# Kernel optimization log

Hardware: AMD Instinct MI355X
Metric: run time of the kernel (lower is better)

## Reference

```python
import jax, jax.numpy as jnp
import numpy as np

SHAPES = np.array([[64, 64], [32, 32], [16, 16], [8, 8]], dtype=np.int64)  # (H_l, W_l)
STARTS = np.array([0, 4096, 5120, 5376], dtype=np.int64)
N_HEADS, N_LEVELS, N_POINTS = 8, 4, 4
NUM_LAYERS, D_MODEL, D_FFN = 6, 256, 1024
B, S = 1, int(SHAPES[:, 0].dot(SHAPES[:, 1]).item()) if False else (1, 5440)[1]
B = 1


def setup_inputs():
    key = jax.random.key(0)
    ks = jax.random.split(key, 16)
    C, F, L = D_MODEL, D_FFN, NUM_LAYERS
    w = lambda k, shape, s: jax.random.normal(k, shape, jnp.float32) * s
    d = {}
    d["src"] = jax.random.normal(ks[0], (B, S, C), jnp.float32)
    d["pos"] = jax.random.normal(ks[1], (B, S, C), jnp.float32) * 0.1
    d["valid_ratios"] = jnp.ones((B, N_LEVELS, 2), jnp.float32)
    d["spatial_shapes"] = jnp.asarray(SHAPES)
    d["level_start_index"] = jnp.asarray(STARTS)
    d["Wv"] = w(ks[2], (L, C, C), 0.03); d["bv"] = jnp.zeros((L, C), jnp.float32)
    d["Woff"] = w(ks[3], (L, C, N_HEADS * N_LEVELS * N_POINTS * 2), 0.002)
    d["boff"] = w(ks[4], (L, N_HEADS * N_LEVELS * N_POINTS * 2), 0.5)
    d["Wattn"] = w(ks[5], (L, C, N_HEADS * N_LEVELS * N_POINTS), 0.02)
    d["battn"] = jnp.zeros((L, N_HEADS * N_LEVELS * N_POINTS), jnp.float32)
    d["Wout"] = w(ks[6], (L, C, C), 0.03); d["bout"] = jnp.zeros((L, C), jnp.float32)
    d["ln1_g"] = jnp.ones((L, C), jnp.float32); d["ln1_b"] = jnp.zeros((L, C), jnp.float32)
    d["W1"] = w(ks[7], (L, C, F), 0.03); d["b1"] = jnp.zeros((L, F), jnp.float32)
    d["W2"] = w(ks[8], (L, F, C), 0.03); d["b2"] = jnp.zeros((L, C), jnp.float32)
    d["ln2_g"] = jnp.ones((L, C), jnp.float32); d["ln2_b"] = jnp.zeros((L, C), jnp.float32)
    return d


def layer_norm(x, g, b, eps=1e-5):
    m = jnp.mean(x, -1, keepdims=True)
    v = jnp.mean(jnp.square(x - m), -1, keepdims=True)
    return (x - m) * jax.lax.rsqrt(v + eps) * g + b


def get_reference_points(valid_ratios):
    # returns [B, S, L, 2] (x, y) normalized coords, matching the TF while-loop
    refs = []
    for l in range(N_LEVELS):
        H, W = int(SHAPES[l, 0]), int(SHAPES[l, 1])
        ry = jnp.linspace(0.5, H - 0.5, H)
        rx = jnp.linspace(0.5, W - 0.5, W)
        yy, xx = jnp.meshgrid(ry, rx, indexing='ij')
        yn = yy.reshape(-1)[None, :] / (valid_ratios[:, l, 0:1] * H)
        xn = xx.reshape(-1)[None, :] / (valid_ratios[:, l, 1:2] * W)
        refs.append(jnp.stack([xn, yn], -1))  # [B, H*W, 2]
    ref = jnp.concatenate(refs, axis=1)       # [B, S, 2]
    vr_wh = valid_ratios[:, None, :, ::-1]    # [B, 1, L, 2] -> (w, h)
    return ref[:, :, None, :] * vr_wh


def bilinear_sample(v_l, loc, Hl, Wl):
    # v_l: [B, Hl*Wl, nH, Dh]; loc: [B, S, nH, P, 2] in [0,1] coords
    # grid_sample align_corners=False, zero padding: pix = loc*size - 0.5
    x = loc[..., 0] * Wl - 0.5
    y = loc[..., 1] * Hl - 0.5
    x0 = jnp.floor(x); y0 = jnp.floor(y)
    lx = x - x0; ly = y - y0
    x0i = x0.astype(jnp.int32); y0i = y0.astype(jnp.int32)
    b_idx = jnp.arange(v_l.shape[0])[:, None, None, None]
    h_idx = jnp.arange(v_l.shape[2])[None, None, :, None]

    def gather(xi, yi):
        valid = (xi >= 0) & (xi < Wl) & (yi >= 0) & (yi < Hl)
        idx = jnp.clip(yi, 0, Hl - 1) * Wl + jnp.clip(xi, 0, Wl - 1)
        v = v_l[b_idx, idx, h_idx, :]  # [B,S,nH,P,Dh]
        return v * valid[..., None].astype(v.dtype)

    v00 = gather(x0i, y0i); v01 = gather(x0i + 1, y0i)
    v10 = gather(x0i, y0i + 1); v11 = gather(x0i + 1, y0i + 1)
    w00 = (1 - lx) * (1 - ly); w01 = lx * (1 - ly)
    w10 = (1 - lx) * ly; w11 = lx * ly
    return (v00 * w00[..., None] + v01 * w01[..., None]
            + v10 * w10[..., None] + v11 * w11[..., None])


def msda(query, src, ref, Wv, bv, Woff, boff, Wattn, battn, Wout, bout):
    Bq, Sq, C = src.shape
    Dh = C // N_HEADS
    value = (src @ Wv + bv).reshape(Bq, Sq, N_HEADS, Dh)
    off = (query @ Woff + boff).reshape(Bq, Sq, N_HEADS, N_LEVELS, N_POINTS, 2)
    aw = jax.nn.softmax((query @ Wattn + battn)
                        .reshape(Bq, Sq, N_HEADS, N_LEVELS * N_POINTS), -1)
    aw = aw.reshape(Bq, Sq, N_HEADS, N_LEVELS, N_POINTS)
    normalizer = jnp.asarray(SHAPES[:, ::-1].copy(), jnp.float32)  # [L,2]=(W,H)
    loc = ref[:, :, None, :, None, :] + off / normalizer[None, None, None, :, None, :]
    out = jnp.zeros((Bq, Sq, N_HEADS, Dh), value.dtype)
    for l in range(N_LEVELS):
        Hl, Wl = int(SHAPES[l, 0]), int(SHAPES[l, 1])
        s0 = int(STARTS[l])
        v_l = value[:, s0:s0 + Hl * Wl]
        sampled = bilinear_sample(v_l, loc[:, :, :, l], Hl, Wl)  # [B,S,nH,P,Dh]
        out = out + jnp.einsum('bshpd,bshp->bshd', sampled, aw[:, :, :, l])
    return out.reshape(Bq, Sq, C) @ Wout + bout


def reference(src, pos, valid_ratios, spatial_shapes, level_start_index,
              Wv, bv, Woff, boff, Wattn, battn, Wout, bout,
              ln1_g, ln1_b, W1, b1, W2, b2, ln2_g, ln2_b):
    ref = get_reference_points(valid_ratios)
    x = src
    for i in range(NUM_LAYERS):
        a = msda(x + pos, x, ref, Wv[i], bv[i], Woff[i], boff[i],
                 Wattn[i], battn[i], Wout[i], bout[i])
        x = layer_norm(x + a, ln1_g[i], ln1_b[i])
        f = jax.nn.relu(x @ W1[i] + b1[i]) @ W2[i] + b2[i]
        x = layer_norm(x + f, ln2_g[i], ln2_b[i])
    return x
```

## Files before the change

### kernel.cpp

```cpp
#include <hip/hip_runtime.h>
#include <hip/hip_bf16.h>

#define S_TOT 5440
#define C_DIM 256
#define F_DIM 1024
#define N_LAYERS 6

__device__ __constant__ int c_HW[4]    = {64, 32, 16, 8};
__device__ __constant__ int c_logW[4]  = {6, 5, 4, 3};
__device__ __constant__ int c_start[4] = {0, 4096, 5120, 5376};

typedef __attribute__((ext_vector_type(8))) short bf16x8;
typedef __attribute__((ext_vector_type(4))) float f32x4;
typedef __attribute__((ext_vector_type(4))) unsigned int u32x4;

__device__ __forceinline__ short f2bf(float f) {
    __hip_bfloat16 h = __float2bfloat16(f);
    return *reinterpret_cast<short*>(&h);
}
union uf32 { unsigned int u; float f; };
__device__ __forceinline__ float lo_f(unsigned int u) { uf32 c; c.u = u << 16;          return c.f; }
__device__ __forceinline__ float hi_f(unsigned int u) { uf32 c; c.u = u & 0xffff0000u; return c.f; }

__global__ __launch_bounds__(256) void prep_weights(
    const float* __restrict__ Wv, const float* __restrict__ Woff,
    const float* __restrict__ Wattn, const float* __restrict__ Wout,
    const float* __restrict__ W1, const float* __restrict__ W2,
    unsigned short* __restrict__ WT)
{
    __shared__ short T[64][72];
    const int bid = blockIdx.x;
    const int layer = bid / 184;
    const int r = bid % 184;
    const float* src; unsigned short* dst; int K, N, kb, nb;
    if (r < 16)       { src = Wv    + (long)layer*65536;  dst = WT + 0       + (long)layer*65536;  K=256;  N=256;  kb=r&3;        nb=r>>2; }
    else if (r < 32)  { src = Woff  + (long)layer*65536;  dst = WT + 393216  + (long)layer*65536;  K=256;  N=256;  kb=(r-16)&3;   nb=(r-16)>>2; }
    else if (r < 40)  { src = Wattn + (long)layer*32768;  dst = WT + 786432  + (long)layer*32768;  K=256;  N=128;  kb=(r-32)&3;   nb=(r-32)>>2; }
    else if (r < 56)  { src = Wout  + (long)layer*65536;  dst = WT + 983040  + (long)layer*65536;  K=256;  N=256;  kb=(r-40)&3;   nb=(r-40)>>2; }
    else if (r < 120) { src = W1    + (long)layer*262144; dst = WT + 1376256 + (long)layer*262144; K=256;  N=1024; kb=(r-56)&3;   nb=(r-56)>>2; }
    else              { src = W2    + (long)layer*262144; dst = WT + 2949120 + (long)layer*262144; K=1024; N=256;  kb=(r-120)&15; nb=(r-120)>>4; }
    const int k0 = kb * 64, n0 = nb * 64;
    const int t = threadIdx.x;
    {
        const int row = t >> 2, cg = (t & 3) * 16;
        const float* sp = src + (long)(k0 + row) * N + n0 + cg;
        float4 v0 = *(const float4*)sp;
        float4 v1 = *(const float4*)(sp + 4);
        float4 v2 = *(const float4*)(sp + 8);
        float4 v3 = *(const float4*)(sp + 12);
        short tmp[16];
        tmp[0]=f2bf(v0.x); tmp[1]=f2bf(v0.y); tmp[2]=f2bf(v0.z); tmp[3]=f2bf(v0.w);
        tmp[4]=f2bf(v1.x); tmp[5]=f2bf(v1.y); tmp[6]=f2bf(v1.z); tmp[7]=f2bf(v1.w);
        tmp[8]=f2bf(v2.x); tmp[9]=f2bf(v2.y); tmp[10]=f2bf(v2.z); tmp[11]=f2bf(v2.w);
        tmp[12]=f2bf(v3.x); tmp[13]=f2bf(v3.y); tmp[14]=f2bf(v3.z); tmp[15]=f2bf(v3.w);
        *(bf16x8*)&T[row][cg]     = *(bf16x8*)&tmp[0];
        *(bf16x8*)&T[row][cg + 8] = *(bf16x8*)&tmp[8];
    }
    __syncthreads();
    {
        const int n = t >> 2, kg = (t & 3) * 16;
        short o[16];
        #pragma unroll
        for (int j = 0; j < 16; ++j) o[j] = T[kg + j][n];
        unsigned short* dp = dst + (long)(n0 + n) * K + k0 + kg;
        *(bf16x8*)dp       = *(bf16x8*)&o[0];
        *(bf16x8*)(dp + 8) = *(bf16x8*)&o[8];
    }
}

__device__ __forceinline__ void prep_A(
    const float* __restrict__ Ain, const float* __restrict__ g,
    const float* __restrict__ b, const float* __restrict__ pos,
    float* __restrict__ xout, int mBase, int doLN,
    short (*As)[264])
{
    const int t = threadIdx.x;
    const int row = t >> 2, q4 = t & 3;
    const long gbase = (long)(mBase + row) * 256 + q4 * 64;
    float va[64];
    #pragma unroll
    for (int j = 0; j < 16; ++j) {
        float4 v = *(const float4*)(Ain + gbase + j * 4);
        va[j*4+0] = v.x; va[j*4+1] = v.y; va[j*4+2] = v.z; va[j*4+3] = v.w;
    }
    if (doLN) {
        float s1 = 0.f, s2 = 0.f;
        #pragma unroll
        for (int j = 0; j < 64; ++j) { s1 += va[j]; s2 += va[j] * va[j]; }
        s1 += __shfl_xor(s1, 1); s2 += __shfl_xor(s2, 1);
        s1 += __shfl_xor(s1, 2); s2 += __shfl_xor(s2, 2);
        const float mean = s1 * (1.f / 256.f);
        const float var  = s2 * (1.f / 256.f) - mean * mean;
        const float rstd = rsqrtf(var + 1e-5f);
        #pragma unroll
        for (int j = 0; j < 16; ++j) {
            float4 g4 = *(const float4*)(g + q4 * 64 + j * 4);
            float4 b4 = *(const float4*)(b + q4 * 64 + j * 4);
            va[j*4+0] = (va[j*4+0] - mean) * rstd * g4.x + b4.x;
            va[j*4+1] = (va[j*4+1] - mean) * rstd * g4.y + b4.y;
            va[j*4+2] = (va[j*4+2] - mean) * rstd * g4.z + b4.z;
            va[j*4+3] = (va[j*4+3] - mean) * rstd * g4.w + b4.w;
        }
    }
    if (xout) {
        #pragma unroll
        for (int j = 0; j < 16; ++j) {
            float4 v;
            v.x = va[j*4+0]; v.y = va[j*4+1]; v.z = va[j*4+2]; v.w = va[j*4+3];
            *(float4*)(xout + gbase + j * 4) = v;
        }
    }
    if (pos) {
        #pragma unroll
        for (int j = 0; j < 16; ++j) {
            float4 p = *(const float4*)(pos + gbase + j * 4);
            va[j*4+0] += p.x; va[j*4+1] += p.y; va[j*4+2] += p.z; va[j*4+3] += p.w;
        }
    }
    #pragma unroll
    for (int j8 = 0; j8 < 8; ++j8) {
        short tmp[8];
        #pragma unroll
        for (int e = 0; e < 8; ++e) tmp[e] = f2bf(va[j8 * 8 + e]);
        *(bf16x8*)&As[row][q4 * 64 + j8 * 8] = *(bf16x8*)tmp;
    }
}

template<int NF>
__device__ __forceinline__ void core_Alds(
    const unsigned short* __restrict__ Bt, int nBase,
    const short (*As)[264], short (*Bs)[72], f32x4 (&acc)[2][NF])
{
    const int t = threadIdx.x;
    const int lane = t & 63, wave = t >> 6;
    const int wr = wave >> 1, wc = wave & 1;
    const int lr = lane & 15;

    #pragma unroll
    for (int i = 0; i < 2; ++i)
        #pragma unroll
        for (int j = 0; j < NF; ++j)
            acc[i][j] = (f32x4){0.f, 0.f, 0.f, 0.f};

    for (int k0 = 0; k0 < 256; k0 += 64) {
        bf16x8 rb[NF];
        #pragma unroll
        for (int q = 0; q < NF; ++q) {
            int flat = q * 256 + t, row = flat >> 3, cg = (flat & 7) * 8;
            rb[q] = *(const bf16x8*)(Bt + (long)(nBase + row) * 256 + k0 + cg);
        }
        __syncthreads();
        #pragma unroll
        for (int q = 0; q < NF; ++q) {
            int flat = q * 256 + t, row = flat >> 3, cg = (flat & 7) * 8;
            *(bf16x8*)&Bs[row][cg] = rb[q];
        }
        __syncthreads();
        #pragma unroll
        for (int kk = 0; kk < 2; ++kk) {
            const int lks = kk * 32 + (lane >> 4) * 8;
            bf16x8 af[2], bfr[NF];
            #pragma unroll
            for (int fm = 0; fm < 2; ++fm)
                af[fm] = *(const bf16x8*)&As[wr * 32 + fm * 16 + lr][k0 + lks];
            #pragma unroll
            for (int fn = 0; fn < NF; ++fn)
                bfr[fn] = *(bf16x8*)&Bs[wc * (NF * 16) + fn * 16 + lr][lks];
            #pragma unroll
            for (int fm = 0; fm < 2; ++fm)
                #pragma unroll
                for (int fn = 0; fn < NF; ++fn)
                    acc[fm][fn] = __builtin_amdgcn_mfma_f32_16x16x32_bf16(
                        af[fm], bfr[fn], acc[fm][fn], 0, 0, 0);
        }
    }
}

template<int NF>
__device__ __forceinline__ void gemm_core(
    const unsigned short* __restrict__ A, const unsigned short* __restrict__ Bt,
    int K, int mBase, int nBase, short (*As)[72], short (*Bs)[72],
    f32x4 (&acc)[2][NF])
{
    const int t = threadIdx.x;
    const int lane = t & 63, wave = t >> 6;
    const int wr = wave >> 1, wc = wave & 1;
    const int lr = lane & 15;

    #pragma unroll
    for (int i = 0; i < 2; ++i)
        #pragma unroll
        for (int j = 0; j < NF; ++j)
            acc[i][j] = (f32x4){0.f, 0.f, 0.f, 0.f};

    for (int k0 = 0; k0 < K; k0 += 64) {
        bf16x8 ra[2], rb[NF];
        #pragma unroll
        for (int q = 0; q < 2; ++q) {
            int flat = q * 256 + t, row = flat >> 3, cg = (flat & 7) * 8;
            ra[q] = *(const bf16x8*)(A + (long)(mBase + row) * K + k0 + cg);
        }
        #pragma unroll
        for (int q = 0; q < NF; ++q) {
            int flat = q * 256 + t, row = flat >> 3, cg = (flat & 7) * 8;
            rb[q] = *(const bf16x8*)(Bt + (long)(nBase + row) * K + k0 + cg);
        }
        __syncthreads();
        #pragma unroll
        for (int q = 0; q < 2; ++q) {
            int flat = q * 256 + t, row = flat >> 3, cg = (flat & 7) * 8;
            *(bf16x8*)&As[row][cg] = ra[q];
        }
        #pragma unroll
        for (int q = 0; q < NF; ++q) {
            int flat = q * 256 + t, row = flat >> 3, cg = (flat & 7) * 8;
            *(bf16x8*)&Bs[row][cg] = rb[q];
        }
        __syncthreads();
        #pragma unroll
        for (int kk = 0; kk < 2; ++kk) {
            const int lks = kk * 32 + (lane >> 4) * 8;
            bf16x8 af[2], bfr[NF];
            #pragma unroll
            for (int fm = 0; fm < 2; ++fm)
                af[fm] = *(bf16x8*)&As[wr * 32 + fm * 16 + lr][lks];
            #pragma unroll
            for (int fn = 0; fn < NF; ++fn)
                bfr[fn] = *(bf16x8*)&Bs[wc * (NF * 16) + fn * 16 + lr][lks];
            #pragma unroll
            for (int fm = 0; fm < 2; ++fm)
                #pragma unroll
                for (int fn = 0; fn < NF; ++fn)
                    acc[fm][fn] = __builtin_amdgcn_mfma_f32_16x16x32_bf16(
                        af[fm], bfr[fn], acc[fm][fn], 0, 0, 0);
        }
    }
}

__global__ __launch_bounds__(256) void proj_ln(
    const float* __restrict__ Ain, const float* __restrict__ pos,
    const float* __restrict__ g, const float* __restrict__ b,
    const unsigned short* __restrict__ WvT, const float* __restrict__ bv,
    const unsigned short* __restrict__ WofT, const float* __restrict__ bof,
    const unsigned short* __restrict__ WatT, const float* __restrict__ bat,
    unsigned short* __restrict__ value_bf, float* __restrict__ offraw,
    float* __restrict__ logits, float* __restrict__ xcur, int doLN)
{
    __shared__ short As[64][264];
    __shared__ short Bs[128][72];
    const int ny = blockIdx.y, mBase = blockIdx.x * 64;
    const unsigned short* Bp; const float* bias; int nBase, kind;
    if (ny < 2)      { Bp = WvT;  bias = bv;  nBase = ny * 128;       kind = 0; }
    else if (ny < 4) { Bp = WofT; bias = bof; nBase = (ny - 2) * 128; kind = 1; }
    else             { Bp = WatT; bias = bat; nBase = 0;              kind = 2; }

    prep_A(Ain, g, b, (kind > 0) ? pos : nullptr,
           (doLN && ny == 0) ? xcur : nullptr, mBase, doLN, As);

    f32x4 acc[2][4];
    core_Alds<4>(Bp, nBase, As, Bs, acc);

    const int lane = threadIdx.x & 63, wave = threadIdx.x >> 6;
    const int wr = wave >> 1, wc = wave & 1;
    #pragma unroll
    for (int fm = 0; fm < 2; ++fm)
        #pragma unroll
        for (int fn = 0; fn < 4; ++fn)
            #pragma unroll
            for (int r = 0; r < 4; ++r) {
                int m = mBase + wr * 32 + fm * 16 + (lane >> 4) * 4 + r;
                int n = nBase + wc * 64 + fn * 16 + (lane & 15);
                float v = acc[fm][fn][r] + bias[n];
                if (kind == 0)      value_bf[(long)m * 256 + n] = (unsigned short)f2bf(v);
                else if (kind == 1) offraw[(long)m * 256 + n] = v;
                else                logits[(long)m * 128 + n] = v;
            }
}

__global__ __launch_bounds__(256) void gemm_w1ln(
    const float* __restrict__ Ain, const float* __restrict__ g,
    const float* __restrict__ b, const unsigned short* __restrict__ W1T,
    const float* __restrict__ bias, unsigned short* __restrict__ hbuf,
    float* __restrict__ xout)
{
    __shared__ short As[64][264];
    __shared__ short Bs[128][72];
    const int mBase = blockIdx.x * 64, nBase = blockIdx.y * 128;

    prep_A(Ain, g, b, nullptr, (blockIdx.y == 0) ? xout : nullptr, mBase, 1, As);

    f32x4 acc[2][4];
    core_Alds<4>(W1T, nBase, As, Bs, acc);

    const int lane = threadIdx.x & 63, wave = threadIdx.x >> 6;
    const int wr = wave >> 1, wc = wave & 1;
    #pragma unroll
    for (int fm = 0; fm < 2; ++fm)
        #pragma unroll
        for (int fn = 0; fn < 4; ++fn)
            #pragma unroll
            for (int r = 0; r < 4; ++r) {
                int m = mBase + wr * 32 + fm * 16 + (lane >> 4) * 4 + r;
                int n = nBase + wc * 64 + fn * 16 + (lane & 15);
                float v = fmaxf(acc[fm][fn][r] + bias[n], 0.f);
                hbuf[(long)m * 1024 + n] = (unsigned short)f2bf(v);
            }
}

__global__ __launch_bounds__(256) void gemm_res(
    const unsigned short* __restrict__ A, const unsigned short* __restrict__ Bt,
    const float* __restrict__ bias, const float* __restrict__ res,
    float* __restrict__ out, int K)
{
    __shared__ short As[64][72];
    __shared__ short Bs[64][72];
    const int mBase = blockIdx.x * 64, nBase = blockIdx.y * 64;
    f32x4 acc[2][2];
    gemm_core<2>(A, Bt, K, mBase, nBase, As, Bs, acc);

    const int lane = threadIdx.x & 63, wave = threadIdx.x >> 6;
    const int wr = wave >> 1, wc = wave & 1;
    #pragma unroll
    for (int fm = 0; fm < 2; ++fm)
        #pragma unroll
        for (int fn = 0; fn < 2; ++fn)
            #pragma unroll
            for (int r = 0; r < 4; ++r) {
                int m = mBase + wr * 32 + fm * 16 + (lane >> 4) * 4 + r;
                int n = nBase + wc * 32 + fn * 16 + (lane & 15);
                out[(long)m * 256 + n] = acc[fm][fn][r] + bias[n] + res[(long)m * 256 + n];
            }
}

__global__ __launch_bounds__(256) void msda2(
    const unsigned short* __restrict__ value, const float* __restrict__ offraw,
    const float* __restrict__ logits, const float* __restrict__ vr,
    unsigned short* __restrict__ outB)
{
    const int t = threadIdx.x;
    const int q = t >> 7, tt = t & 127;
    const int s = blockIdx.x * 2 + q;

    __shared__ int4   sIdx[2][128];
    __shared__ float4 sW[2][128];

    {
        const int pt = tt & 15, l = pt >> 2;

        float lg = logits[(long)s * 128 + tt];
        float m = lg;
        #pragma unroll
        for (int o = 1; o < 16; o <<= 1) m = fmaxf(m, __shfl_xor(m, o));
        float e = expf(lg - m);
        float sum = e;
        #pragma unroll
        for (int o = 1; o < 16; o <<= 1) sum += __shfl_xor(sum, o);
        float aw = e / sum;

        int ls = (s < 4096) ? 0 : (s < 5120) ? 1 : (s < 5376) ? 2 : 3;
        int lw = c_logW[ls];
        int Wq = c_HW[ls];
        int rem = s - c_start[ls];
        int qi = rem >> lw, qj = rem & (Wq - 1);
        float xh = (qj + 0.5f) / (vr[ls * 2 + 1] * (float)Wq);
        float yh = (qi + 0.5f) / (vr[ls * 2 + 0] * (float)Wq);

        const int Wl = c_HW[l], sl = c_start[l];
        const float fW = (float)Wl;
        float refx = xh * vr[l * 2 + 1];
        float refy = yh * vr[l * 2 + 0];
        float2 oxy = *(const float2*)(offraw + (long)s * 256 + tt * 2);
        float x = refx * fW + oxy.x - 0.5f;
        float y = refy * fW + oxy.y - 0.5f;
        float x0f = floorf(x), y0f = floorf(y);
        float fx = x - x0f, fy = y - y0f;
        int x0 = (int)x0f, y0 = (int)y0f;
        int x1 = x0 + 1, y1 = y0 + 1;
        float vx0 = (x0 >= 0 && x0 < Wl) ? 1.f : 0.f;
        float vx1 = (x1 >= 0 && x1 < Wl) ? 1.f : 0.f;
        float vy0 = (y0 >= 0 && y0 < Wl) ? 1.f : 0.f;
        float vy1 = (y1 >= 0 && y1 < Wl) ? 1.f : 0.f;
        int cx0 = min(max(x0, 0), Wl - 1), cx1 = min(max(x1, 0), Wl - 1);
        int cy0 = min(max(y0, 0), Wl - 1), cy1 = min(max(y1, 0), Wl - 1);

        int4 id4;
        id4.x = sl + cy0 * Wl + cx0;
        id4.y = sl + cy0 * Wl + cx1;
        id4.z = sl + cy1 * Wl + cx0;
        id4.w = sl + cy1 * Wl + cx1;
        sIdx[q][tt] = id4;
        float4 w4;
        w4.x = aw * (1.f - fx) * (1.f - fy) * vx0 * vy0;
        w4.y = aw * fx * (1.f - fy) * vx1 * vy0;
        w4.z = aw * (1.f - fx) * fy * vx0 * vy1;
        w4.w = aw * fx * fy * vx1 * vy1;
        sW[q][tt] = w4;
    }
    __syncthreads();

    const int h = tt >> 4, pg = (tt >> 2) & 3, dq = tt & 3;
    const int cb = h * 32 + dq * 8;

    float a8[8] = {0.f,0.f,0.f,0.f,0.f,0.f,0.f,0.f};
    #pragma unroll
    for (int p = 0; p < 4; ++p) {
        const int ei = h * 16 + pg * 4 + p;
        int4 id = sIdx[q][ei];
        float4 w = sW[q][ei];
        u32x4 u0 = *(const u32x4*)(value + (long)id.x * 256 + cb);
        u32x4 u1 = *(const u32x4*)(value + (long)id.y * 256 + cb);
        u32x4 u2 = *(const u32x4*)(value + (long)id.z * 256 + cb);
        u32x4 u3 = *(const u32x4*)(value + (long)id.w * 256 + cb);
        #pragma unroll
        for (int j = 0; j < 4; ++j) {
            a8[2*j]   += w.x * lo_f(u0[j]) + w.y * lo_f(u1[j])
                       + w.z * lo_f(u2[j]) + w.w * lo_f(u3[j]);
            a8[2*j+1] += w.x * hi_f(u0[j]) + w.y * hi_f(u1[j])
                       + w.z * hi_f(u2[j]) + w.w * hi_f(u3[j]);
        }
    }
    #pragma unroll
    for (int j = 0; j < 8; ++j) {
        a8[j] += __shfl_xor(a8[j], 4);
        a8[j] += __shfl_xor(a8[j], 8);
    }
    if (pg == 0) {
        short o8[8];
        #pragma unroll
        for (int j = 0; j < 8; ++j) o8[j] = f2bf(a8[j]);
        *(bf16x8*)(outB + (long)s * 256 + cb) = *(bf16x8*)o8;
    }
}

__global__ __launch_bounds__(256) void ln4f(
    const float* __restrict__ in, const float* __restrict__ g,
    const float* __restrict__ b, float* __restrict__ out)
{
    const int wave = threadIdx.x >> 6, lane = threadIdx.x & 63;
    const int s = blockIdx.x * 4 + wave;
    f32x4 v = *(const f32x4*)(in + (long)s * 256 + lane * 4);

    float sum = v[0] + v[1] + v[2] + v[3];
    #pragma unroll
    for (int o = 1; o < 64; o <<= 1) sum += __shfl_xor(sum, o);
    const float mean = sum * (1.f / 256.f);

    f32x4 d = v - mean;
    float sq = d[0]*d[0] + d[1]*d[1] + d[2]*d[2] + d[3]*d[3];
    #pragma unroll
    for (int o = 1; o < 64; o <<= 1) sq += __shfl_xor(sq, o);
    const float rstd = rsqrtf(sq * (1.f / 256.f) + 1e-5f);

    f32x4 gg = *(const f32x4*)(g + lane * 4);
    f32x4 bb = *(const f32x4*)(b + lane * 4);
    f32x4 o4 = d * rstd * gg + bb;
    *(f32x4*)(out + (long)s * 256 + lane * 4) = o4;
}

extern "C" void kernel_launch(void* const* d_in, const int* in_sizes, int n_in,
                              void* d_out, int out_size, void* d_ws, size_t ws_size,
                              hipStream_t stream) {
    const float* src   = (const float*)d_in[0];
    const float* pos   = (const float*)d_in[1];
    const float* vr    = (const float*)d_in[2];
    const float* Wv    = (const float*)d_in[5];
    const float* bv    = (const float*)d_in[6];
    const float* Woff  = (const float*)d_in[7];
    const float* boff  = (const float*)d_in[8];
    const float* Wattn = (const float*)d_in[9];
    const float* battn = (const float*)d_in[10];
    const float* Wout  = (const float*)d_in[11];
    const float* bout  = (const float*)d_in[12];
    const float* ln1g  = (const float*)d_in[13];
    const float* ln1b  = (const float*)d_in[14];
    const float* W1    = (const float*)d_in[15];
    const float* b1    = (const float*)d_in[16];
    const float* W2    = (const float*)d_in[17];
    const float* b2    = (const float*)d_in[18];
    const float* ln2g  = (const float*)d_in[19];
    const float* ln2b  = (const float*)d_in[20];

    const int S = S_TOT, C = C_DIM;
    const long SC = (long)S * C;

    float* ws     = (float*)d_ws;
    float* tmp2   = ws;
    float* xcur   = tmp2 + SC;
    float* offraw = xcur + SC;
    float* logits = offraw + SC;
    unsigned short* value_bf = (unsigned short*)(logits + (long)S * 128);
    unsigned short* msda_bf  = value_bf + SC;
    unsigned short* hbuf_bf  = msda_bf + SC;
    unsigned short* WT       = hbuf_bf + (long)S * F_DIM;

    float* xln1 = offraw;

    const unsigned short* WvT  = WT + 0;
    const unsigned short* WofT = WT + 393216;
    const unsigned short* WatT = WT + 786432;
    const unsigned short* WouT = WT + 983040;
    const unsigned short* W1T  = WT + 1376256;
    const unsigned short* W2T  = WT + 2949120;

    prep_weights<<<1104, 256, 0, stream>>>(Wv, Woff, Wattn, Wout, W1, W2, WT);

    for (int i = 0; i < N_LAYERS; ++i) {
        const float* Ain = (i == 0) ? src : tmp2;
        const float* g2  = (i == 0) ? nullptr : ln2g + (long)(i - 1) * C;
        const float* bb2 = (i == 0) ? nullptr : ln2b + (long)(i - 1) * C;
        const float* resWout = (i == 0) ? src : xcur;

        proj_ln<<<dim3(85, 5), 256, 0, stream>>>(
            Ain, pos, g2, bb2,
            WvT + (long)i * 65536, bv + (long)i * C,
            WofT + (long)i * 65536, boff + (long)i * 256,
            WatT + (long)i * 32768, battn + (long)i * 128,
            value_bf, offraw, logits, xcur, (i == 0) ? 0 : 1);

        msda2<<<S / 2, 256, 0, stream>>>(value_bf, offraw, logits, vr, msda_bf);

        gemm_res<<<dim3(85, 4), 256, 0, stream>>>(
            msda_bf, WouT + (long)i * 65536, bout + (long)i * C, resWout, tmp2, 256);

        gemm_w1ln<<<dim3(85, 8), 256, 0, stream>>>(
            tmp2, ln1g + (long)i * C, ln1b + (long)i * C,
            W1T + (long)i * 262144, b1 + (long)i * F_DIM, hbuf_bf, xln1);

        gemm_res<<<dim3(85, 4), 256, 0, stream>>>(
            hbuf_bf, W2T + (long)i * 262144, b2 + (long)i * C, xln1, tmp2, 1024);
    }

    ln4f<<<S / 4, 256, 0, stream>>>(
        tmp2, ln2g + (long)(N_LAYERS - 1) * C, ln2b + (long)(N_LAYERS - 1) * C,
        (float*)d_out);
}
```

Baseline: 503.5 us.

## Store offsets and logits in bf16 and widen W1 GEMM tile to 256 columns

The projection kernel now writes sampling offsets and attention logits as bf16 instead of fp32, and the sampling kernel reads them back with bit-shift conversions. This halves the memory traffic for those intermediates, at the cost of lower precision in the sampling offsets. Separately, the W1 GEMM tile grows from 128 to 256 columns, which halves the grid and the redundant LayerNorm prep of the A tile. The larger tile raises registers and LDS per block, which may reduce occupancy. The workspace is re-laid out so xln1 has its own buffer instead of aliasing offraw.

```diff
diff --git a/kernel.cpp b/kernel.cpp
--- a/kernel.cpp
+++ b/kernel.cpp
@@ -21,6 +21,7 @@
 union uf32 { unsigned int u; float f; };
 __device__ __forceinline__ float lo_f(unsigned int u) { uf32 c; c.u = u << 16;          return c.f; }
 __device__ __forceinline__ float hi_f(unsigned int u) { uf32 c; c.u = u & 0xffff0000u; return c.f; }
+__device__ __forceinline__ float bf2f(unsigned short u) { uf32 c; c.u = ((unsigned int)u) << 16; return c.f; }
 
 __global__ __launch_bounds__(256) void prep_weights(
     const float* __restrict__ Wv, const float* __restrict__ Woff,
@@ -243,8 +244,8 @@
     const unsigned short* __restrict__ WvT, const float* __restrict__ bv,
     const unsigned short* __restrict__ WofT, const float* __restrict__ bof,
     const unsigned short* __restrict__ WatT, const float* __restrict__ bat,
-    unsigned short* __restrict__ value_bf, float* __restrict__ offraw,
-    float* __restrict__ logits, float* __restrict__ xcur, int doLN)
+    unsigned short* __restrict__ value_bf, unsigned short* __restrict__ offraw,
+    unsigned short* __restrict__ logits, float* __restrict__ xcur, int doLN)
 {
     __shared__ short As[64][264];
     __shared__ short Bs[128][72];
@@ -272,8 +273,8 @@
                 int n = nBase + wc * 64 + fn * 16 + (lane & 15);
                 float v = acc[fm][fn][r] + bias[n];
                 if (kind == 0)      value_bf[(long)m * 256 + n] = (unsigned short)f2bf(v);
-                else if (kind == 1) offraw[(long)m * 256 + n] = v;
-                else                logits[(long)m * 128 + n] = v;
+                else if (kind == 1) offraw[(long)m * 256 + n] = (unsigned short)f2bf(v);
+                else                logits[(long)m * 128 + n] = (unsigned short)f2bf(v);
             }
 }
 
@@ -284,24 +285,24 @@
     float* __restrict__ xout)
 {
     __shared__ short As[64][264];
-    __shared__ short Bs[128][72];
-    const int mBase = blockIdx.x * 64, nBase = blockIdx.y * 128;
+    __shared__ short Bs[256][72];
+    const int mBase = blockIdx.x * 64, nBase = blockIdx.y * 256;
 
     prep_A(Ain, g, b, nullptr, (blockIdx.y == 0) ? xout : nullptr, mBase, 1, As);
 
-    f32x4 acc[2][4];
-    core_Alds<4>(W1T, nBase, As, Bs, acc);
+    f32x4 acc[2][8];
+    core_Alds<8>(W1T, nBase, As, Bs, acc);
 
     const int lane = threadIdx.x & 63, wave = threadIdx.x >> 6;
     const int wr = wave >> 1, wc = wave & 1;
     #pragma unroll
     for (int fm = 0; fm < 2; ++fm)
         #pragma unroll
-        for (int fn = 0; fn < 4; ++fn)
+        for (int fn = 0; fn < 8; ++fn)
             #pragma unroll
             for (int r = 0; r < 4; ++r) {
                 int m = mBase + wr * 32 + fm * 16 + (lane >> 4) * 4 + r;
-                int n = nBase + wc * 64 + fn * 16 + (lane & 15);
+                int n = nBase + wc * 128 + fn * 16 + (lane & 15);
                 float v = fmaxf(acc[fm][fn][r] + bias[n], 0.f);
                 hbuf[(long)m * 1024 + n] = (unsigned short)f2bf(v);
             }
@@ -333,8 +334,8 @@
 }
 
 __global__ __launch_bounds__(256) void msda2(
-    const unsigned short* __restrict__ value, const float* __restrict__ offraw,
-    const float* __restrict__ logits, const float* __restrict__ vr,
+    const unsigned short* __restrict__ value, const unsigned short* __restrict__ offraw,
+    const unsigned short* __restrict__ logits, const float* __restrict__ vr,
     unsigned short* __restrict__ outB)
 {
     const int t = threadIdx.x;
@@ -347,7 +348,7 @@
     {
         const int pt = tt & 15, l = pt >> 2;
 
-        float lg = logits[(long)s * 128 + tt];
+        float lg = bf2f(logits[(long)s * 128 + tt]);
         float m = lg;
         #pragma unroll
         for (int o = 1; o < 16; o <<= 1) m = fmaxf(m, __shfl_xor(m, o));
@@ -369,9 +370,10 @@
         const float fW = (float)Wl;
         float refx = xh * vr[l * 2 + 1];
         float refy = yh * vr[l * 2 + 0];
-        float2 oxy = *(const float2*)(offraw + (long)s * 256 + tt * 2);
-        float x = refx * fW + oxy.x - 0.5f;
-        float y = refy * fW + oxy.y - 0.5f;
+        unsigned int uoxy = *(const unsigned int*)(offraw + (long)s * 256 + tt * 2);
+        float ox = lo_f(uoxy), oy = hi_f(uoxy);
+        float x = refx * fW + ox - 0.5f;
+        float y = refy * fW + oy - 0.5f;
         float x0f = floorf(x), y0f = floorf(y);
         float fx = x - x0f, fy = y - y0f;
         int x0 = (int)x0f, y0 = (int)y0f;
@@ -486,14 +488,13 @@
     float* ws     = (float*)d_ws;
     float* tmp2   = ws;
     float* xcur   = tmp2 + SC;
-    float* offraw = xcur + SC;
-    float* logits = offraw + SC;
-    unsigned short* value_bf = (unsigned short*)(logits + (long)S * 128);
-    unsigned short* msda_bf  = value_bf + SC;
-    unsigned short* hbuf_bf  = msda_bf + SC;
-    unsigned short* WT       = hbuf_bf + (long)S * F_DIM;
-
-    float* xln1 = offraw;
+    float* xln1   = xcur + SC;
+    unsigned short* offraw_bf = (unsigned short*)(xln1 + SC);
+    unsigned short* logits_bf = offraw_bf + SC;
+    unsigned short* value_bf  = logits_bf + (long)S * 128;
+    unsigned short* msda_bf   = value_bf + SC;
+    unsigned short* hbuf_bf   = msda_bf + SC;
+    unsigned short* WT        = hbuf_bf + (long)S * F_DIM;
 
     const unsigned short* WvT  = WT + 0;
     const unsigned short* WofT = WT + 393216;
@@ -515,14 +516,14 @@
             WvT + (long)i * 65536, bv + (long)i * C,
             WofT + (long)i * 65536, boff + (long)i * 256,
             WatT + (long)i * 32768, battn + (long)i * 128,
-            value_bf, offraw, logits, xcur, (i == 0) ? 0 : 1);
-
-        msda2<<<S / 2, 256, 0, stream>>>(value_bf, offraw, logits, vr, msda_bf);
+            value_bf, offraw_bf, logits_bf, xcur, (i == 0) ? 0 : 1);
+
+        msda2<<<S / 2, 256, 0, stream>>>(value_bf, offraw_bf, logits_bf, vr, msda_bf);
 
         gemm_res<<<dim3(85, 4), 256, 0, stream>>>(
             msda_bf, WouT + (long)i * 65536, bout + (long)i * C, resWout, tmp2, 256);
 
-        gemm_w1ln<<<dim3(85, 8), 256, 0, stream>>>(
+        gemm_w1ln<<<dim3(85, 4), 256, 0, stream>>>(
             tmp2, ln1g + (long)i * C, ln1b + (long)i * C,
             W1T + (long)i * 262144, b1 + (long)i * F_DIM, hbuf_bf, xln1);
 
```

Result: faster. 466.1 us (-7.4%).
